# Kernel optimization log

Measured on AMD Instinct MI355X. Metric: run time of the kernel, lower is better.

The kernel has to match this reference:

```python
import jax, jax.numpy as jnp
import numpy as np

B, L, F = 8, 1024, 128
D = 256          # d_model (intermediate_representation)
DI = 512         # d_inner = expand * d_model
N = 32           # d_state
K = 4            # d_conv
R = 16           # dt_rank = ceil(d_model/16)
NC = 2           # n_class


def setup_inputs() -> dict:
    key = jax.random.key(0)
    ks = jax.random.split(key, 12)
    s = 0.02
    return {
        "x": jax.random.normal(ks[0], (B, L, F), jnp.float32),
        "W1": jax.random.normal(ks[1], (D, F), jnp.float32) * s,
        "b1": jnp.zeros((D,), jnp.float32),
        "ln_g": jnp.ones((D,), jnp.float32),
        "ln_b": jnp.zeros((D,), jnp.float32),
        "in_proj_w": jax.random.normal(ks[2], (2 * DI, D), jnp.float32) * s,
        "conv_w": jax.random.normal(ks[3], (DI, K), jnp.float32) * s,
        "conv_b": jnp.zeros((DI,), jnp.float32),
        "x_proj_w": jax.random.normal(ks[4], (R + 2 * N, DI), jnp.float32) * s,
        "dt_proj_w": jax.random.normal(ks[5], (DI, R), jnp.float32) * s,
        "dt_proj_b": jax.random.normal(ks[6], (DI,), jnp.float32) * 0.5,
        "A_log": jnp.log(jnp.broadcast_to(jnp.arange(1, N + 1, dtype=jnp.float32), (DI, N))),
        "D_param": jnp.ones((DI,), jnp.float32),
        "out_proj_w": jax.random.normal(ks[7], (D, DI), jnp.float32) * s,
        "W_out": jax.random.normal(ks[8], (NC, D), jnp.float32) * s,
        "b_out": jnp.zeros((NC,), jnp.float32),
    }


def _mamba(u, in_proj_w, conv_w, conv_b, x_proj_w, dt_proj_w, dt_proj_b, A_log, D_param, out_proj_w):
    # u: (B, L, D)
    xz = u @ in_proj_w.T                      # (B, L, 2*DI)
    xi, z = jnp.split(xz, 2, axis=-1)         # each (B, L, DI)
    # depthwise causal conv1d, kernel K
    xc = jnp.transpose(xi, (0, 2, 1))         # (B, DI, L)
    xc = jax.lax.conv_general_dilated(
        xc, conv_w[:, None, :], (1,), [(K - 1, 0)],
        dimension_numbers=("NCH", "OIH", "NCH"), feature_group_count=DI)
    xi = jnp.transpose(xc, (0, 2, 1)) + conv_b
    xi = jax.nn.silu(xi)
    dbc = xi @ x_proj_w.T                     # (B, L, R+2N)
    dt, Bm, Cm = jnp.split(dbc, [R, R + N], axis=-1)
    delta = jax.nn.softplus(dt @ dt_proj_w.T + dt_proj_b)   # (B, L, DI)
    A = -jnp.exp(A_log)                       # (DI, N)
    dA = jnp.exp(delta[..., None] * A)        # (B, L, DI, N)
    dBu = delta[..., None] * Bm[:, :, None, :] * xi[..., None]  # (B, L, DI, N)

    def step(h, t):
        dA_t, dBu_t, C_t = t
        h = dA_t * h + dBu_t                  # (B, DI, N)
        y = jnp.einsum("bdn,bn->bd", h, C_t)
        return h, y

    h0 = jnp.zeros((u.shape[0], DI, N), u.dtype)
    _, ys = jax.lax.scan(step, h0, (jnp.swapaxes(dA, 0, 1), jnp.swapaxes(dBu, 0, 1), jnp.swapaxes(Cm, 0, 1)))
    y = jnp.swapaxes(ys, 0, 1) + xi * D_param # (B, L, DI)
    y = y * jax.nn.silu(z)
    return y @ out_proj_w.T                   # (B, L, D)


def reference(x, W1, b1, ln_g, ln_b, in_proj_w, conv_w, conv_b, x_proj_w,
              dt_proj_w, dt_proj_b, A_log, D_param, out_proj_w, W_out, b_out):
    h = x @ W1.T + b1                         # (B, L, D)
    mu = jnp.mean(h, -1, keepdims=True)
    var = jnp.var(h, -1, keepdims=True)
    h = (h - mu) / jnp.sqrt(var + 1e-5) * ln_g + ln_b
    h = jax.nn.relu(h)
    h = _mamba(h, in_proj_w, conv_w, conv_b, x_proj_w, dt_proj_w, dt_proj_b,
               A_log, D_param, out_proj_w)
    return h @ W_out.T + b_out                # (B, L, NC)
```

## Files before the change

kernel.cpp:

```cpp
#include <hip/hip_runtime.h>
#include <math.h>

#define BB 8
#define LL 1024
#define FF 128
#define DD 256
#define DIN 512
#define NSTATE 32
#define KCONV 4
#define RNK 16
#define NCLS 2
#define NROWS (BB*LL)
#define NCH 32
#define TCH 32
#define XKS 4
#define XKC (DIN/XKS)

__device__ __forceinline__ unsigned short f2bf(float f) {
  unsigned int x = __float_as_uint(f);
  unsigned int r = (x + 0x7fffu + ((x >> 16) & 1u)) >> 16;
  return (unsigned short)r;
}
__device__ __forceinline__ float bf2f(unsigned short u) {
  return __uint_as_float((unsigned int)u << 16);
}
__device__ __forceinline__ void split_bf(float x, unsigned short& h,
                                         unsigned short& l) {
  h = f2bf(x);
  float hf = __uint_as_float((unsigned int)h << 16);
  l = f2bf(x - hf);
}

typedef __attribute__((ext_vector_type(8))) short frag8;
typedef __attribute__((ext_vector_type(4))) float f32x4;

__global__ __launch_bounds__(256) void head_kernel(
    const float* __restrict__ x, const float* __restrict__ W1,
    const float* __restrict__ b1, const float* __restrict__ ln_g,
    const float* __restrict__ ln_b, unsigned short* __restrict__ u_bf,
    const float* __restrict__ in_proj_w, unsigned short* __restrict__ W_bf,
    const float* __restrict__ W_out, const float* __restrict__ opw,
    float* __restrict__ Wc, const float* __restrict__ xpw,
    unsigned short* __restrict__ xpw_h, unsigned short* __restrict__ xpw_l)
{
  const int blk = blockIdx.x;
  const int tid = threadIdx.x;
  if (blk >= 256) {
    if (blk < 512) {
      int i = (blk - 256) * 256 + tid;
      float4 v = ((const float4*)in_proj_w)[i];
      ushort4 o;
      o.x = f2bf(v.x); o.y = f2bf(v.y); o.z = f2bf(v.z); o.w = f2bf(v.w);
      ((ushort4*)W_bf)[i] = o;
    } else if (blk < 516) {
      int idx = (blk - 512) * 256 + tid;
      int c = idx >> 9;
      int d = idx & (DIN - 1);
      float acc = 0.f;
      for (int j = 0; j < DD; j++)
        acc = fmaf(W_out[c * DD + j], opw[j * DIN + d], acc);
      Wc[idx] = acc;
    } else {
      int i = (blk - 516) * 256 + tid;
      float4 v = ((const float4*)xpw)[i];
      ushort4 hi, lo;
      split_bf(v.x, hi.x, lo.x);
      split_bf(v.y, hi.y, lo.y);
      split_bf(v.z, hi.z, lo.z);
      split_bf(v.w, hi.w, lo.w);
      ((ushort4*)xpw_h)[i] = hi;
      ((ushort4*)xpw_l)[i] = lo;
    }
    return;
  }

  constexpr int BM = 32, BK = 32, K = FF;
  __shared__ __align__(16) unsigned short Ah[BM][40];
  __shared__ __align__(16) unsigned short Al[BM][40];
  __shared__ __align__(16) unsigned short Bh[DD][40];
  __shared__ __align__(16) unsigned short Bl[DD][40];
  __shared__ float srow[2][BM];
  __shared__ float s2row[2][BM];
  const int bm = blk * BM;
  const int wave = tid >> 6;
  const int lane = tid & 63;
  const int lm = lane & 15, quad = lane >> 4;
  const int msub = wave & 1;
  const int ch = wave >> 1;

  f32x4 acc[8];
  #pragma unroll
  for (int j = 0; j < 8; j++) acc[j] = (f32x4){0.f, 0.f, 0.f, 0.f};

  for (int k0 = 0; k0 < K; k0 += BK) {
    {
      int row = tid >> 3, seg = (tid & 7) << 2;
      float4 v = *(const float4*)(x + (size_t)(bm + row) * K + k0 + seg);
      split_bf(v.x, Ah[row][seg + 0], Al[row][seg + 0]);
      split_bf(v.y, Ah[row][seg + 1], Al[row][seg + 1]);
      split_bf(v.z, Ah[row][seg + 2], Al[row][seg + 2]);
      split_bf(v.w, Ah[row][seg + 3], Al[row][seg + 3]);
    }
    #pragma unroll
    for (int it = 0; it < 8; it++) {
      int q = it * 256 + tid;
      int row = q >> 3, seg = (q & 7) << 2;
      float4 v = *(const float4*)(W1 + (size_t)row * K + k0 + seg);
      split_bf(v.x, Bh[row][seg + 0], Bl[row][seg + 0]);
      split_bf(v.y, Bh[row][seg + 1], Bl[row][seg + 1]);
      split_bf(v.z, Bh[row][seg + 2], Bl[row][seg + 2]);
      split_bf(v.w, Bh[row][seg + 3], Bl[row][seg + 3]);
    }
    __syncthreads();
    frag8 ah = *(const frag8*)&Ah[msub * 16 + lm][quad * 8];
    frag8 al = *(const frag8*)&Al[msub * 16 + lm][quad * 8];
    #pragma unroll
    for (int j = 0; j < 8; j++) {
      frag8 bh = *(const frag8*)&Bh[ch * 128 + j * 16 + lm][quad * 8];
      frag8 bl = *(const frag8*)&Bl[ch * 128 + j * 16 + lm][quad * 8];
      acc[j] = __builtin_amdgcn_mfma_f32_16x16x32_bf16(ah, bh, acc[j], 0, 0, 0);
      acc[j] = __builtin_amdgcn_mfma_f32_16x16x32_bf16(ah, bl, acc[j], 0, 0, 0);
      acc[j] = __builtin_amdgcn_mfma_f32_16x16x32_bf16(al, bh, acc[j], 0, 0, 0);
    }
    __syncthreads();
  }

  float b1v[8];
  #pragma unroll
  for (int j = 0; j < 8; j++) b1v[j] = b1[ch * 128 + j * 16 + lm];
  #pragma unroll
  for (int r = 0; r < 4; r++) {
    float s = 0.f, s2 = 0.f;
    #pragma unroll
    for (int j = 0; j < 8; j++) {
      float v = acc[j][r] + b1v[j];
      s += v; s2 = fmaf(v, v, s2);
    }
    s  += __shfl_xor(s, 1);  s  += __shfl_xor(s, 2);
    s  += __shfl_xor(s, 4);  s  += __shfl_xor(s, 8);
    s2 += __shfl_xor(s2, 1); s2 += __shfl_xor(s2, 2);
    s2 += __shfl_xor(s2, 4); s2 += __shfl_xor(s2, 8);
    if (lm == 0) {
      srow[ch][msub * 16 + quad * 4 + r] = s;
      s2row[ch][msub * 16 + quad * 4 + r] = s2;
    }
  }
  __syncthreads();

  float gv[8], bv[8];
  #pragma unroll
  for (int j = 0; j < 8; j++) {
    gv[j] = ln_g[ch * 128 + j * 16 + lm];
    bv[j] = ln_b[ch * 128 + j * 16 + lm];
  }
  #pragma unroll
  for (int r = 0; r < 4; r++) {
    int row32 = msub * 16 + quad * 4 + r;
    float st  = srow[0][row32] + srow[1][row32];
    float s2t = s2row[0][row32] + s2row[1][row32];
    float mean = st * (1.f / DD);
    float var  = s2t * (1.f / DD) - mean * mean;
    float rstd = rsqrtf(var + 1e-5f);
    size_t gr = (size_t)(bm + row32) * DD + ch * 128 + lm;
    #pragma unroll
    for (int j = 0; j < 8; j++) {
      float v = acc[j][r] + b1v[j];
      float o = (v - mean) * rstd * gv[j] + bv[j];
      u_bf[gr + j * 16] = f2bf(o > 0.f ? o : 0.f);
    }
  }
}

__global__ __launch_bounds__(256) void inproj_mfma(
    const unsigned short* __restrict__ A,
    const unsigned short* __restrict__ Bw,
    float* __restrict__ xbuf,
    unsigned short* __restrict__ zbuf)
{
  constexpr int K = DD;
  constexpr int BM = 128, BN = 128, BK = 32;
  __shared__ __align__(16) unsigned short As[BM * BK];
  __shared__ __align__(16) unsigned short Bs[BN * BK];
  const int tid = threadIdx.x;
  const int bm = blockIdx.y * BM;
  const int bn = blockIdx.x * BN;
  const int wave = tid >> 6;
  const int lane = tid & 63;
  const int wm = (wave >> 1) * 64;
  const int wn = (wave & 1) * 64;
  const int lm = lane & 15;
  const int quad = lane >> 4;

  f32x4 acc[4][4];
  #pragma unroll
  for (int i = 0; i < 4; i++)
    #pragma unroll
    for (int j = 0; j < 4; j++)
      acc[i][j] = (f32x4){0.f, 0.f, 0.f, 0.f};

  for (int k0 = 0; k0 < K; k0 += BK) {
    int idx = tid;
    #pragma unroll
    for (int it = 0; it < 2; it++, idx += 256) {
      int row = idx >> 2, seg = (idx & 3) * 8;
      *(uint4*)&As[row * BK + seg] =
          *(const uint4*)&A[(size_t)(bm + row) * K + k0 + seg];
      *(uint4*)&Bs[row * BK + seg] =
          *(const uint4*)&Bw[(size_t)(bn + row) * K + k0 + seg];
    }
    __syncthreads();
    frag8 af[4], bfr[4];
    #pragma unroll
    for (int i = 0; i < 4; i++)
      af[i] = *(const frag8*)&As[(wm + i * 16 + lm) * BK + quad * 8];
    #pragma unroll
    for (int j = 0; j < 4; j++)
      bfr[j] = *(const frag8*)&Bs[(wn + j * 16 + lm) * BK + quad * 8];
    #pragma unroll
    for (int i = 0; i < 4; i++)
      #pragma unroll
      for (int j = 0; j < 4; j++)
        acc[i][j] = __builtin_amdgcn_mfma_f32_16x16x32_bf16(
            af[i], bfr[j], acc[i][j], 0, 0, 0);
    __syncthreads();
  }

  if (bn < DIN) {
    #pragma unroll
    for (int i = 0; i < 4; i++) {
      #pragma unroll
      for (int r = 0; r < 4; r++) {
        int gm = bm + wm + i * 16 + quad * 4 + r;
        float* crow = xbuf + (size_t)gm * DIN + bn + wn + lm;
        #pragma unroll
        for (int j = 0; j < 4; j++)
          crow[j * 16] = acc[i][j][r];
      }
    }
  } else {
    #pragma unroll
    for (int i = 0; i < 4; i++) {
      #pragma unroll
      for (int r = 0; r < 4; r++) {
        int gm = bm + wm + i * 16 + quad * 4 + r;
        unsigned short* zrow = zbuf + (size_t)gm * DIN + (bn - DIN) + wn + lm;
        #pragma unroll
        for (int j = 0; j < 4; j++)
          zrow[j * 16] = f2bf(acc[i][j][r]);
      }
    }
  }
}

__global__ __launch_bounds__(256) void xproj_mfma(
    const float* __restrict__ xbuf, const float* __restrict__ cw,
    const float* __restrict__ cb, const unsigned short* __restrict__ xpw_h,
    const unsigned short* __restrict__ xpw_l,
    float* __restrict__ part, unsigned short* __restrict__ xi_bf)
{
  constexpr int BM = 64;
  __shared__ __align__(16) unsigned short Ah[BM][40];
  __shared__ __align__(16) unsigned short Al[BM][40];
  __shared__ __align__(16) unsigned short Bh[80][40];
  __shared__ __align__(16) unsigned short Bl[80][40];
  const int tid = threadIdx.x;
  const int bm = blockIdx.x * BM;
  const int ks = blockIdx.y;
  const int kb = ks * XKC;
  const int wave = tid >> 6;
  const int lane = tid & 63;
  const int lm = lane & 15, quad = lane >> 4;

  f32x4 acc[5];
  #pragma unroll
  for (int n = 0; n < 5; n++) acc[n] = (f32x4){0.f, 0.f, 0.f, 0.f};

  for (int k0 = 0; k0 < XKC; k0 += 32) {
    for (int q = tid; q < BM * 8; q += 256) {
      int row = q >> 3, seg = (q & 7) << 2;
      int gr = bm + row;
      int l = gr & (LL - 1);
      int dcol = kb + k0 + seg;
      const float* bp = xbuf + (size_t)gr * DIN + dcol;
      float4 c0 = ((const float4*)cw)[dcol + 0];
      float4 c1 = ((const float4*)cw)[dcol + 1];
      float4 c2 = ((const float4*)cw)[dcol + 2];
      float4 c3 = ((const float4*)cw)[dcol + 3];
      float4 a = ((const float4*)cb)[dcol >> 2];
      #pragma unroll
      for (int k = 0; k < KCONV; k++) {
        int lk = l - (KCONV - 1) + k;
        if (lk >= 0) {
          float4 v = *(const float4*)(bp + (ptrdiff_t)(k - (KCONV - 1)) * DIN);
          a.x = fmaf((&c0.x)[k], v.x, a.x);
          a.y = fmaf((&c1.x)[k], v.y, a.y);
          a.z = fmaf((&c2.x)[k], v.z, a.z);
          a.w = fmaf((&c3.x)[k], v.w, a.w);
        }
      }
      float4 r;
      r.x = a.x * (1.f / (1.f + __expf(-a.x)));
      r.y = a.y * (1.f / (1.f + __expf(-a.y)));
      r.z = a.z * (1.f / (1.f + __expf(-a.z)));
      r.w = a.w * (1.f / (1.f + __expf(-a.w)));
      ushort4 xb;
      split_bf(r.x, Ah[row][seg + 0], Al[row][seg + 0]);
      split_bf(r.y, Ah[row][seg + 1], Al[row][seg + 1]);
      split_bf(r.z, Ah[row][seg + 2], Al[row][seg + 2]);
      split_bf(r.w, Ah[row][seg + 3], Al[row][seg + 3]);
      xb.x = Ah[row][seg + 0]; xb.y = Ah[row][seg + 1];
      xb.z = Ah[row][seg + 2]; xb.w = Ah[row][seg + 3];
      *(ushort4*)&xi_bf[(size_t)gr * DIN + dcol] = xb;
    }
    for (int q = tid; q < 80 * 8; q += 256) {
      int row = q >> 3, seg = (q & 7) << 2;
      int g = row * DIN + kb + k0 + seg;
      *(ushort4*)&Bh[row][seg] = *(const ushort4*)&xpw_h[g];
      *(ushort4*)&Bl[row][seg] = *(const ushort4*)&xpw_l[g];
    }
    __syncthreads();
    frag8 ah = *(const frag8*)&Ah[wave * 16 + lm][quad * 8];
    frag8 al = *(const frag8*)&Al[wave * 16 + lm][quad * 8];
    #pragma unroll
    for (int n = 0; n < 5; n++) {
      frag8 bh = *(const frag8*)&Bh[n * 16 + lm][quad * 8];
      frag8 bl = *(const frag8*)&Bl[n * 16 + lm][quad * 8];
      acc[n] = __builtin_amdgcn_mfma_f32_16x16x32_bf16(ah, bh, acc[n], 0, 0, 0);
      acc[n] = __builtin_amdgcn_mfma_f32_16x16x32_bf16(ah, bl, acc[n], 0, 0, 0);
      acc[n] = __builtin_amdgcn_mfma_f32_16x16x32_bf16(al, bh, acc[n], 0, 0, 0);
    }
    __syncthreads();
  }
  #pragma unroll
  for (int n = 0; n < 5; n++) {
    #pragma unroll
    for (int r = 0; r < 4; r++) {
      int gm = bm + wave * 16 + quad * 4 + r;
      part[((size_t)ks * NROWS + gm) * 80 + n * 16 + lm] = acc[n][r];
    }
  }
}

__device__ __forceinline__ float softplus_f(float v) {
  return (v > 20.f) ? v : __logf(1.f + __expf(v));
}

__device__ __forceinline__ void pow_tree(float e1, float* base,
                                         float& e8, float& e16, float& e24) {
  float e2 = e1 * e1;
  float e4 = e2 * e2;
  e8 = e4 * e4;
  e16 = e8 * e8;
  e24 = e16 * e8;
  base[0] = e1;       base[1] = e2;       base[2] = e2 * e1;  base[3] = e4;
  base[4] = e4 * e1;  base[5] = e4 * e2;  base[6] = e4 * base[2]; base[7] = e8;
}

__global__ __launch_bounds__(256) void scan_p1(
    const float* __restrict__ xpart, const unsigned short* __restrict__ xi_bf,
    const float* __restrict__ A_log,
    const float* __restrict__ wdt_g, const float* __restrict__ bdt_g,
    unsigned short* __restrict__ hend, float* __restrict__ sdb,
    float* __restrict__ xsum)
{
  const int blk = blockIdx.x;
  const int half = blk & 1;
  const int c = (blk >> 1) & (NCH - 1);
  const int b = blk >> 6;
  const int tid = threadIdx.x;
  const int d = half * 256 + tid;

  __shared__ float sdbc[TCH * 80];
  {
    const size_t tb = ((size_t)b * LL + c * TCH) * 20;
    const float4* p0 = (const float4*)xpart + tb;
    const float4* p1 = p0 + (size_t)NROWS * 20;
    const float4* p2 = p1 + (size_t)NROWS * 20;
    const float4* p3 = p2 + (size_t)NROWS * 20;
    float4* dst = (float4*)sdbc;
    float4* xs  = (float4*)xsum + tb;
    for (int q = tid; q < TCH * 20; q += 256) {
      float4 a = p0[q], e = p1[q], f = p2[q], g = p3[q];
      float4 o;
      o.x = (a.x + e.x) + (f.x + g.x);
      o.y = (a.y + e.y) + (f.y + g.y);
      o.z = (a.z + e.z) + (f.z + g.z);
      o.w = (a.w + e.w) + (f.w + g.w);
      dst[q] = o;
      if (half == 0) xs[q] = o;
    }
  }

  float h[NSTATE], wdt[16];
  const float A1 = -__expf(A_log[d * NSTATE]);
  #pragma unroll
  for (int n = 0; n < NSTATE; n++) h[n] = 0.f;
  {
    const float4* wp = (const float4*)(wdt_g + d * 16);
    #pragma unroll
    for (int k = 0; k < 4; k++) {
      float4 w = wp[k];
      wdt[4*k+0] = w.x; wdt[4*k+1] = w.y; wdt[4*k+2] = w.z; wdt[4*k+3] = w.w;
    }
  }
  const float bdt = bdt_g[d];
  __syncthreads();

  float sd = 0.f;
  const size_t rowbase = (size_t)b * LL + c * TCH;
  const size_t xib = rowbase * DIN + d;
  float xv_a = bf2f(xi_bf[xib]);
  float xv_b = bf2f(xi_bf[xib + DIN]);
  #pragma unroll 4
  for (int t = 0; t < TCH; t++) {
    float xv = xv_a;
    xv_a = xv_b;
    xv_b = (t + 2 < TCH) ? bf2f(xi_bf[xib + (size_t)(t + 2) * DIN]) : 0.f;
    const float* row = sdbc + t * 80;
    float d0 = bdt, d1 = 0.f, d2 = 0.f, d3 = 0.f;
    #pragma unroll
    for (int j = 0; j < 4; j++) {
      d0 = fmaf(row[j],      wdt[j],      d0);
      d1 = fmaf(row[j + 4],  wdt[j + 4],  d1);
      d2 = fmaf(row[j + 8],  wdt[j + 8],  d2);
      d3 = fmaf(row[j + 12], wdt[j + 12], d3);
    }
    float dtv = (d0 + d1) + (d2 + d3);
    float dlt = softplus_f(dtv);
    float dxv = dlt * xv;
    sd += dlt;
    float base[8], e8, e16, e24;
    pow_tree(__expf(dlt * A1), base, e8, e16, e24);
    #pragma unroll
    for (int k = 0; k < 8; k++) {
      h[k]      = fmaf(base[k],       h[k],      dxv * row[RNK + k]);
      h[k + 8]  = fmaf(base[k] * e8,  h[k + 8],  dxv * row[RNK + k + 8]);
      h[k + 16] = fmaf(base[k] * e16, h[k + 16], dxv * row[RNK + k + 16]);
      h[k + 24] = fmaf(base[k] * e24, h[k + 24], dxv * row[RNK + k + 24]);
    }
  }
  size_t base2 = ((size_t)c * (BB * DIN) + b * DIN + d) * NSTATE;
  ushort4* hv = (ushort4*)(hend + base2);
  #pragma unroll
  for (int k = 0; k < 8; k++) {
    ushort4 o;
    o.x = f2bf(h[4*k]);   o.y = f2bf(h[4*k+1]);
    o.z = f2bf(h[4*k+2]); o.w = f2bf(h[4*k+3]);
    hv[k] = o;
  }
  sdb[c * (BB * DIN) + b * DIN + d] = sd;
}

__global__ __launch_bounds__(256) void scan_p2(
    unsigned short* __restrict__ hend, const float* __restrict__ sdb,
    const float* __restrict__ A_log)
{
  const int idx = blockIdx.x * 256 + threadIdx.x;
  const int n = idx & 31;
  const int pair = idx >> 5;
  const int d = pair & (DIN - 1);
  const float Av = -__expf(A_log[d * NSTATE + n]);
  float h = 0.f;
  size_t off = (size_t)pair * NSTATE + n;
  const size_t stride = (size_t)BB * DIN * NSTATE;
  float he = bf2f(hend[off]);
  float sd = sdb[pair];
  #pragma unroll 1
  for (int c = 0; c < NCH; c++) {
    float he_n = 0.f, sd_n = 0.f;
    if (c + 1 < NCH) {
      he_n = bf2f(hend[off + stride]);
      sd_n = sdb[(size_t)(c + 1) * (BB * DIN) + pair];
    }
    float p = __expf(sd * Av);
    hend[off] = f2bf(h);
    h = fmaf(p, h, he);
    he = he_n; sd = sd_n;
    off += stride;
  }
}

__global__ __launch_bounds__(512) void scan_p3(
    const float* __restrict__ xsum, const unsigned short* __restrict__ xi_bf,
    const unsigned short* __restrict__ zbuf, const float* __restrict__ A_log,
    const float* __restrict__ wdt_g, const float* __restrict__ bdt_g,
    const float* __restrict__ Dp, const float* __restrict__ Wc,
    const float* __restrict__ b_out,
    const unsigned short* __restrict__ hstart, float* __restrict__ out)
{
  const int blk = blockIdx.x;
  const int c = blk & (NCH - 1);
  const int b = blk >> 5;
  const int tid = threadIdx.x;
  const int d = tid;

  __shared__ float sdbc[TCH * 80];
  __shared__ float wcs[2][DIN];
  __shared__ float ymat[16][DIN];
  {
    const size_t tb = ((size_t)b * LL + c * TCH) * 20;
    const float4* p0 = (const float4*)xsum + tb;
    float4* dst = (float4*)sdbc;
    for (int q = tid; q < TCH * 20; q += 512) dst[q] = p0[q];
    wcs[0][tid] = Wc[tid];
    wcs[1][tid] = Wc[DIN + tid];
  }

  float h[NSTATE], wdt[16];
  const float A1 = -__expf(A_log[d * NSTATE]);
  {
    size_t base = ((size_t)c * (BB * DIN) + b * DIN + d) * NSTATE;
    const ushort4* hv = (const ushort4*)(hstart + base);
    #pragma unroll
    for (int k = 0; k < 8; k++) {
      ushort4 v = hv[k];
      h[4*k]   = bf2f(v.x); h[4*k+1] = bf2f(v.y);
      h[4*k+2] = bf2f(v.z); h[4*k+3] = bf2f(v.w);
    }
  }
  {
    const float4* wp = (const float4*)(wdt_g + d * 16);
    #pragma unroll
    for (int k = 0; k < 4; k++) {
      float4 w = wp[k];
      wdt[4*k+0] = w.x; wdt[4*k+1] = w.y; wdt[4*k+2] = w.z; wdt[4*k+3] = w.w;
    }
  }
  const float bdt = bdt_g[d];
  const float Dval = Dp[d];
  __syncthreads();

  const size_t rowbase = (size_t)b * LL + c * TCH;
  const int wave = tid >> 6;
  const int lane = tid & 63;

  #pragma unroll 1
  for (int phase = 0; phase < 2; phase++) {
    const int t0 = phase * 16;
    const size_t xib = (rowbase + t0) * DIN + d;
    float xva = bf2f(xi_bf[xib]);
    float zva = bf2f(zbuf[xib]);
    float xvb = bf2f(xi_bf[xib + DIN]);
    float zvb = bf2f(zbuf[xib + DIN]);
    #pragma unroll 2
    for (int tl = 0; tl < 16; tl++) {
      const int t = t0 + tl;
      float xv = xva, zv = zva;
      xva = xvb; zva = zvb;
      if (tl + 2 < 16) {
        size_t nxt = xib + (size_t)(tl + 2) * DIN;
        xvb = bf2f(xi_bf[nxt]);
        zvb = bf2f(zbuf[nxt]);
      } else { xvb = 0.f; zvb = 0.f; }
      const float* row = sdbc + t * 80;
      float d0 = bdt, d1 = 0.f, d2 = 0.f, d3 = 0.f;
      #pragma unroll
      for (int j = 0; j < 4; j++) {
        d0 = fmaf(row[j],      wdt[j],      d0);
        d1 = fmaf(row[j + 4],  wdt[j + 4],  d1);
        d2 = fmaf(row[j + 8],  wdt[j + 8],  d2);
        d3 = fmaf(row[j + 12], wdt[j + 12], d3);
      }
      float dtv = (d0 + d1) + (d2 + d3);
      float dlt = softplus_f(dtv);
      float dxv = dlt * xv;
      float base[8], e8, e16, e24;
      pow_tree(__expf(dlt * A1), base, e8, e16, e24);
      float yacc = 0.f;
      #pragma unroll
      for (int k = 0; k < 8; k++) {
        h[k]      = fmaf(base[k],       h[k],      dxv * row[RNK + k]);
        h[k + 8]  = fmaf(base[k] * e8,  h[k + 8],  dxv * row[RNK + k + 8]);
        h[k + 16] = fmaf(base[k] * e16, h[k + 16], dxv * row[RNK + k + 16]);
        h[k + 24] = fmaf(base[k] * e24, h[k + 24], dxv * row[RNK + k + 24]);
        yacc = fmaf(h[k],      row[RNK + NSTATE + k],      yacc);
        yacc = fmaf(h[k + 8],  row[RNK + NSTATE + k + 8],  yacc);
        yacc = fmaf(h[k + 16], row[RNK + NSTATE + k + 16], yacc);
        yacc = fmaf(h[k + 24], row[RNK + NSTATE + k + 24], yacc);
      }
      float sg = 1.f / (1.f + __expf(-zv));
      ymat[tl][d] = (yacc + xv * Dval) * (zv * sg);
    }
    __syncthreads();

    #pragma unroll
    for (int i = 0; i < 2; i++) {
      int tl = wave * 2 + i;
      float p0 = 0.f, p1 = 0.f;
      #pragma unroll
      for (int k = 0; k < 8; k++) {
        int dd = lane + k * 64;
        float yv = ymat[tl][dd];
        p0 = fmaf(yv, wcs[0][dd], p0);
        p1 = fmaf(yv, wcs[1][dd], p1);
      }
      #pragma unroll
      for (int off = 32; off > 0; off >>= 1) {
        p0 += __shfl_xor(p0, off);
        p1 += __shfl_xor(p1, off);
      }
      if (lane == 0) {
        out[(rowbase + t0 + tl) * NCLS + 0] = p0 + b_out[0];
        out[(rowbase + t0 + tl) * NCLS + 1] = p1 + b_out[1];
      }
    }
    __syncthreads();
  }
}

extern "C" void kernel_launch(void* const* d_in, const int* in_sizes, int n_in,
                              void* d_out, int out_size, void* d_ws, size_t ws_size,
                              hipStream_t stream)
{
  const float* x         = (const float*)d_in[0];
  const float* W1        = (const float*)d_in[1];
  const float* b1        = (const float*)d_in[2];
  const float* ln_g      = (const float*)d_in[3];
  const float* ln_b      = (const float*)d_in[4];
  const float* in_proj_w = (const float*)d_in[5];
  const float* conv_w    = (const float*)d_in[6];
  const float* conv_b    = (const float*)d_in[7];
  const float* x_proj_w  = (const float*)d_in[8];
  const float* dt_proj_w = (const float*)d_in[9];
  const float* dt_proj_b = (const float*)d_in[10];
  const float* A_log     = (const float*)d_in[11];
  const float* D_param   = (const float*)d_in[12];
  const float* out_proj_w= (const float*)d_in[13];
  const float* W_out     = (const float*)d_in[14];
  const float* b_out     = (const float*)d_in[15];
  float* out = (float*)d_out;

  float* ws   = (float*)d_ws;
  float* xbuf = ws;
  unsigned short* zbuf  = (unsigned short*)(xbuf + (size_t)NROWS * DIN);
  unsigned short* xi_bf = zbuf + (size_t)NROWS * DIN;
  unsigned short* u_bf  = xi_bf + (size_t)NROWS * DIN;
  unsigned short* W_bf  = u_bf + (size_t)NROWS * DD;
  float* Wc    = (float*)(W_bf + 2 * DIN * DD);
  float* sdb   = Wc + 2 * DIN;
  float* xpart = sdb + (size_t)NCH * BB * DIN;
  unsigned short* hend = (unsigned short*)(xpart + (size_t)XKS * NROWS * 80);
  unsigned short* xpw_h = hend + (size_t)NCH * BB * DIN * NSTATE;
  unsigned short* xpw_l = xpw_h + 80 * DIN;
  float* xsum = (float*)(xpw_l + 80 * DIN);

  head_kernel<<<556, 256, 0, stream>>>(x, W1, b1, ln_g, ln_b, u_bf,
                                       in_proj_w, W_bf, W_out, out_proj_w, Wc,
                                       x_proj_w, xpw_h, xpw_l);

  inproj_mfma<<<dim3(8, 64), 256, 0, stream>>>(u_bf, W_bf, xbuf, zbuf);

  xproj_mfma<<<dim3(NROWS / 64, XKS), 256, 0, stream>>>(xbuf, conv_w, conv_b,
                                                        xpw_h, xpw_l, xpart, xi_bf);

  scan_p1<<<BB * NCH * 2, 256, 0, stream>>>(xpart, xi_bf, A_log, dt_proj_w,
                                            dt_proj_b, hend, sdb, xsum);
  scan_p2<<<(BB * DIN * NSTATE) / 256, 256, 0, stream>>>(hend, sdb, A_log);
  scan_p3<<<BB * NCH, 512, 0, stream>>>(xsum, xi_bf, zbuf, A_log, dt_proj_w,
                                        dt_proj_b, D_param, Wc, b_out, hend, out);
}
```

Before: 211.7 us.

## Fuse all six stage kernels into one cooperative persistent kernel with grid syncs

Replaces the separate head, in-projection, x-projection and three scan kernels with one cooperative kernel of 256 blocks of 512 threads. Stages are separated by grid.sync, and each stage uses its own view of a shared-memory union. The goal is to remove the launch gaps and tail effects between the six kernels. In exchange, every stage is forced onto a fixed 256-block grid, so the GEMM stages may lose occupancy and parallelism, and grid-wide barriers add their own cost.

```diff
diff --git a/kernel.cpp b/kernel.cpp
--- a/kernel.cpp
+++ b/kernel.cpp
@@ -1,5 +1,8 @@
 #include <hip/hip_runtime.h>
+#include <hip/hip_cooperative_groups.h>
 #include <math.h>
+
+namespace cg = cooperative_groups;
 
 #define BB 8
 #define LL 1024
@@ -34,313 +37,6 @@
 typedef __attribute__((ext_vector_type(8))) short frag8;
 typedef __attribute__((ext_vector_type(4))) float f32x4;
 
-__global__ __launch_bounds__(256) void head_kernel(
-    const float* __restrict__ x, const float* __restrict__ W1,
-    const float* __restrict__ b1, const float* __restrict__ ln_g,
-    const float* __restrict__ ln_b, unsigned short* __restrict__ u_bf,
-    const float* __restrict__ in_proj_w, unsigned short* __restrict__ W_bf,
-    const float* __restrict__ W_out, const float* __restrict__ opw,
-    float* __restrict__ Wc, const float* __restrict__ xpw,
-    unsigned short* __restrict__ xpw_h, unsigned short* __restrict__ xpw_l)
-{
-  const int blk = blockIdx.x;
-  const int tid = threadIdx.x;
-  if (blk >= 256) {
-    if (blk < 512) {
-      int i = (blk - 256) * 256 + tid;
-      float4 v = ((const float4*)in_proj_w)[i];
-      ushort4 o;
-      o.x = f2bf(v.x); o.y = f2bf(v.y); o.z = f2bf(v.z); o.w = f2bf(v.w);
-      ((ushort4*)W_bf)[i] = o;
-    } else if (blk < 516) {
-      int idx = (blk - 512) * 256 + tid;
-      int c = idx >> 9;
-      int d = idx & (DIN - 1);
-      float acc = 0.f;
-      for (int j = 0; j < DD; j++)
-        acc = fmaf(W_out[c * DD + j], opw[j * DIN + d], acc);
-      Wc[idx] = acc;
-    } else {
-      int i = (blk - 516) * 256 + tid;
-      float4 v = ((const float4*)xpw)[i];
-      ushort4 hi, lo;
-      split_bf(v.x, hi.x, lo.x);
-      split_bf(v.y, hi.y, lo.y);
-      split_bf(v.z, hi.z, lo.z);
-      split_bf(v.w, hi.w, lo.w);
-      ((ushort4*)xpw_h)[i] = hi;
-      ((ushort4*)xpw_l)[i] = lo;
-    }
-    return;
-  }
-
-  constexpr int BM = 32, BK = 32, K = FF;
-  __shared__ __align__(16) unsigned short Ah[BM][40];
-  __shared__ __align__(16) unsigned short Al[BM][40];
-  __shared__ __align__(16) unsigned short Bh[DD][40];
-  __shared__ __align__(16) unsigned short Bl[DD][40];
-  __shared__ float srow[2][BM];
-  __shared__ float s2row[2][BM];
-  const int bm = blk * BM;
-  const int wave = tid >> 6;
-  const int lane = tid & 63;
-  const int lm = lane & 15, quad = lane >> 4;
-  const int msub = wave & 1;
-  const int ch = wave >> 1;
-
-  f32x4 acc[8];
-  #pragma unroll
-  for (int j = 0; j < 8; j++) acc[j] = (f32x4){0.f, 0.f, 0.f, 0.f};
-
-  for (int k0 = 0; k0 < K; k0 += BK) {
-    {
-      int row = tid >> 3, seg = (tid & 7) << 2;
-      float4 v = *(const float4*)(x + (size_t)(bm + row) * K + k0 + seg);
-      split_bf(v.x, Ah[row][seg + 0], Al[row][seg + 0]);
-      split_bf(v.y, Ah[row][seg + 1], Al[row][seg + 1]);
-      split_bf(v.z, Ah[row][seg + 2], Al[row][seg + 2]);
-      split_bf(v.w, Ah[row][seg + 3], Al[row][seg + 3]);
-    }
-    #pragma unroll
-    for (int it = 0; it < 8; it++) {
-      int q = it * 256 + tid;
-      int row = q >> 3, seg = (q & 7) << 2;
-      float4 v = *(const float4*)(W1 + (size_t)row * K + k0 + seg);
-      split_bf(v.x, Bh[row][seg + 0], Bl[row][seg + 0]);
-      split_bf(v.y, Bh[row][seg + 1], Bl[row][seg + 1]);
-      split_bf(v.z, Bh[row][seg + 2], Bl[row][seg + 2]);
-      split_bf(v.w, Bh[row][seg + 3], Bl[row][seg + 3]);
-    }
-    __syncthreads();
-    frag8 ah = *(const frag8*)&Ah[msub * 16 + lm][quad * 8];
-    frag8 al = *(const frag8*)&Al[msub * 16 + lm][quad * 8];
-    #pragma unroll
-    for (int j = 0; j < 8; j++) {
-      frag8 bh = *(const frag8*)&Bh[ch * 128 + j * 16 + lm][quad * 8];
-      frag8 bl = *(const frag8*)&Bl[ch * 128 + j * 16 + lm][quad * 8];
-      acc[j] = __builtin_amdgcn_mfma_f32_16x16x32_bf16(ah, bh, acc[j], 0, 0, 0);
-      acc[j] = __builtin_amdgcn_mfma_f32_16x16x32_bf16(ah, bl, acc[j], 0, 0, 0);
-      acc[j] = __builtin_amdgcn_mfma_f32_16x16x32_bf16(al, bh, acc[j], 0, 0, 0);
-    }
-    __syncthreads();
-  }
-
-  float b1v[8];
-  #pragma unroll
-  for (int j = 0; j < 8; j++) b1v[j] = b1[ch * 128 + j * 16 + lm];
-  #pragma unroll
-  for (int r = 0; r < 4; r++) {
-    float s = 0.f, s2 = 0.f;
-    #pragma unroll
-    for (int j = 0; j < 8; j++) {
-      float v = acc[j][r] + b1v[j];
-      s += v; s2 = fmaf(v, v, s2);
-    }
-    s  += __shfl_xor(s, 1);  s  += __shfl_xor(s, 2);
-    s  += __shfl_xor(s, 4);  s  += __shfl_xor(s, 8);
-    s2 += __shfl_xor(s2, 1); s2 += __shfl_xor(s2, 2);
-    s2 += __shfl_xor(s2, 4); s2 += __shfl_xor(s2, 8);
-    if (lm == 0) {
-      srow[ch][msub * 16 + quad * 4 + r] = s;
-      s2row[ch][msub * 16 + quad * 4 + r] = s2;
-    }
-  }
-  __syncthreads();
-
-  float gv[8], bv[8];
-  #pragma unroll
-  for (int j = 0; j < 8; j++) {
-    gv[j] = ln_g[ch * 128 + j * 16 + lm];
-    bv[j] = ln_b[ch * 128 + j * 16 + lm];
-  }
-  #pragma unroll
-  for (int r = 0; r < 4; r++) {
-    int row32 = msub * 16 + quad * 4 + r;
-    float st  = srow[0][row32] + srow[1][row32];
-    float s2t = s2row[0][row32] + s2row[1][row32];
-    float mean = st * (1.f / DD);
-    float var  = s2t * (1.f / DD) - mean * mean;
-    float rstd = rsqrtf(var + 1e-5f);
-    size_t gr = (size_t)(bm + row32) * DD + ch * 128 + lm;
-    #pragma unroll
-    for (int j = 0; j < 8; j++) {
-      float v = acc[j][r] + b1v[j];
-      float o = (v - mean) * rstd * gv[j] + bv[j];
-      u_bf[gr + j * 16] = f2bf(o > 0.f ? o : 0.f);
-    }
-  }
-}
-
-__global__ __launch_bounds__(256) void inproj_mfma(
-    const unsigned short* __restrict__ A,
-    const unsigned short* __restrict__ Bw,
-    float* __restrict__ xbuf,
-    unsigned short* __restrict__ zbuf)
-{
-  constexpr int K = DD;
-  constexpr int BM = 128, BN = 128, BK = 32;
-  __shared__ __align__(16) unsigned short As[BM * BK];
-  __shared__ __align__(16) unsigned short Bs[BN * BK];
-  const int tid = threadIdx.x;
-  const int bm = blockIdx.y * BM;
-  const int bn = blockIdx.x * BN;
-  const int wave = tid >> 6;
-  const int lane = tid & 63;
-  const int wm = (wave >> 1) * 64;
-  const int wn = (wave & 1) * 64;
-  const int lm = lane & 15;
-  const int quad = lane >> 4;
-
-  f32x4 acc[4][4];
-  #pragma unroll
-  for (int i = 0; i < 4; i++)
-    #pragma unroll
-    for (int j = 0; j < 4; j++)
-      acc[i][j] = (f32x4){0.f, 0.f, 0.f, 0.f};
-
-  for (int k0 = 0; k0 < K; k0 += BK) {
-    int idx = tid;
-    #pragma unroll
-    for (int it = 0; it < 2; it++, idx += 256) {
-      int row = idx >> 2, seg = (idx & 3) * 8;
-      *(uint4*)&As[row * BK + seg] =
-          *(const uint4*)&A[(size_t)(bm + row) * K + k0 + seg];
-      *(uint4*)&Bs[row * BK + seg] =
-          *(const uint4*)&Bw[(size_t)(bn + row) * K + k0 + seg];
-    }
-    __syncthreads();
-    frag8 af[4], bfr[4];
-    #pragma unroll
-    for (int i = 0; i < 4; i++)
-      af[i] = *(const frag8*)&As[(wm + i * 16 + lm) * BK + quad * 8];
-    #pragma unroll
-    for (int j = 0; j < 4; j++)
-      bfr[j] = *(const frag8*)&Bs[(wn + j * 16 + lm) * BK + quad * 8];
-    #pragma unroll
-    for (int i = 0; i < 4; i++)
-      #pragma unroll
-      for (int j = 0; j < 4; j++)
-        acc[i][j] = __builtin_amdgcn_mfma_f32_16x16x32_bf16(
-            af[i], bfr[j], acc[i][j], 0, 0, 0);
-    __syncthreads();
-  }
-
-  if (bn < DIN) {
-    #pragma unroll
-    for (int i = 0; i < 4; i++) {
-      #pragma unroll
-      for (int r = 0; r < 4; r++) {
-        int gm = bm + wm + i * 16 + quad * 4 + r;
-        float* crow = xbuf + (size_t)gm * DIN + bn + wn + lm;
-        #pragma unroll
-        for (int j = 0; j < 4; j++)
-          crow[j * 16] = acc[i][j][r];
-      }
-    }
-  } else {
-    #pragma unroll
-    for (int i = 0; i < 4; i++) {
-      #pragma unroll
-      for (int r = 0; r < 4; r++) {
-        int gm = bm + wm + i * 16 + quad * 4 + r;
-        unsigned short* zrow = zbuf + (size_t)gm * DIN + (bn - DIN) + wn + lm;
-        #pragma unroll
-        for (int j = 0; j < 4; j++)
-          zrow[j * 16] = f2bf(acc[i][j][r]);
-      }
-    }
-  }
-}
-
-__global__ __launch_bounds__(256) void xproj_mfma(
-    const float* __restrict__ xbuf, const float* __restrict__ cw,
-    const float* __restrict__ cb, const unsigned short* __restrict__ xpw_h,
-    const unsigned short* __restrict__ xpw_l,
-    float* __restrict__ part, unsigned short* __restrict__ xi_bf)
-{
-  constexpr int BM = 64;
-  __shared__ __align__(16) unsigned short Ah[BM][40];
-  __shared__ __align__(16) unsigned short Al[BM][40];
-  __shared__ __align__(16) unsigned short Bh[80][40];
-  __shared__ __align__(16) unsigned short Bl[80][40];
-  const int tid = threadIdx.x;
-  const int bm = blockIdx.x * BM;
-  const int ks = blockIdx.y;
-  const int kb = ks * XKC;
-  const int wave = tid >> 6;
-  const int lane = tid & 63;
-  const int lm = lane & 15, quad = lane >> 4;
-
-  f32x4 acc[5];
-  #pragma unroll
-  for (int n = 0; n < 5; n++) acc[n] = (f32x4){0.f, 0.f, 0.f, 0.f};
-
-  for (int k0 = 0; k0 < XKC; k0 += 32) {
-    for (int q = tid; q < BM * 8; q += 256) {
-      int row = q >> 3, seg = (q & 7) << 2;
-      int gr = bm + row;
-      int l = gr & (LL - 1);
-      int dcol = kb + k0 + seg;
-      const float* bp = xbuf + (size_t)gr * DIN + dcol;
-      float4 c0 = ((const float4*)cw)[dcol + 0];
-      float4 c1 = ((const float4*)cw)[dcol + 1];
-      float4 c2 = ((const float4*)cw)[dcol + 2];
-      float4 c3 = ((const float4*)cw)[dcol + 3];
-      float4 a = ((const float4*)cb)[dcol >> 2];
-      #pragma unroll
-      for (int k = 0; k < KCONV; k++) {
-        int lk = l - (KCONV - 1) + k;
-        if (lk >= 0) {
-          float4 v = *(const float4*)(bp + (ptrdiff_t)(k - (KCONV - 1)) * DIN);
-          a.x = fmaf((&c0.x)[k], v.x, a.x);
-          a.y = fmaf((&c1.x)[k], v.y, a.y);
-          a.z = fmaf((&c2.x)[k], v.z, a.z);
-          a.w = fmaf((&c3.x)[k], v.w, a.w);
-        }
-      }
-      float4 r;
-      r.x = a.x * (1.f / (1.f + __expf(-a.x)));
-      r.y = a.y * (1.f / (1.f + __expf(-a.y)));
-      r.z = a.z * (1.f / (1.f + __expf(-a.z)));
-      r.w = a.w * (1.f / (1.f + __expf(-a.w)));
-      ushort4 xb;
-      split_bf(r.x, Ah[row][seg + 0], Al[row][seg + 0]);
-      split_bf(r.y, Ah[row][seg + 1], Al[row][seg + 1]);
-      split_bf(r.z, Ah[row][seg + 2], Al[row][seg + 2]);
-      split_bf(r.w, Ah[row][seg + 3], Al[row][seg + 3]);
-      xb.x = Ah[row][seg + 0]; xb.y = Ah[row][seg + 1];
-      xb.z = Ah[row][seg + 2]; xb.w = Ah[row][seg + 3];
-      *(ushort4*)&xi_bf[(size_t)gr * DIN + dcol] = xb;
-    }
-    for (int q = tid; q < 80 * 8; q += 256) {
-      int row = q >> 3, seg = (q & 7) << 2;
-      int g = row * DIN + kb + k0 + seg;
-      *(ushort4*)&Bh[row][seg] = *(const ushort4*)&xpw_h[g];
-      *(ushort4*)&Bl[row][seg] = *(const ushort4*)&xpw_l[g];
-    }
-    __syncthreads();
-    frag8 ah = *(const frag8*)&Ah[wave * 16 + lm][quad * 8];
-    frag8 al = *(const frag8*)&Al[wave * 16 + lm][quad * 8];
-    #pragma unroll
-    for (int n = 0; n < 5; n++) {
-      frag8 bh = *(const frag8*)&Bh[n * 16 + lm][quad * 8];
-      frag8 bl = *(const frag8*)&Bl[n * 16 + lm][quad * 8];
-      acc[n] = __builtin_amdgcn_mfma_f32_16x16x32_bf16(ah, bh, acc[n], 0, 0, 0);
-      acc[n] = __builtin_amdgcn_mfma_f32_16x16x32_bf16(ah, bl, acc[n], 0, 0, 0);
-      acc[n] = __builtin_amdgcn_mfma_f32_16x16x32_bf16(al, bh, acc[n], 0, 0, 0);
-    }
-    __syncthreads();
-  }
-  #pragma unroll
-  for (int n = 0; n < 5; n++) {
-    #pragma unroll
-    for (int r = 0; r < 4; r++) {
-      int gm = bm + wave * 16 + quad * 4 + r;
-      part[((size_t)ks * NROWS + gm) * 80 + n * 16 + lm] = acc[n][r];
-    }
-  }
-}
-
 __device__ __forceinline__ float softplus_f(float v) {
   return (v > 20.f) ? v : __logf(1.f + __expf(v));
 }
@@ -356,203 +52,346 @@
   base[4] = e4 * e1;  base[5] = e4 * e2;  base[6] = e4 * base[2]; base[7] = e8;
 }
 
-__global__ __launch_bounds__(256) void scan_p1(
-    const float* __restrict__ xpart, const unsigned short* __restrict__ xi_bf,
-    const float* __restrict__ A_log,
-    const float* __restrict__ wdt_g, const float* __restrict__ bdt_g,
-    unsigned short* __restrict__ hend, float* __restrict__ sdb,
-    float* __restrict__ xsum)
+struct MegaArgs {
+  const float *x, *W1, *b1, *ln_g, *ln_b, *in_proj_w, *conv_w, *conv_b,
+              *x_proj_w, *dt_proj_w, *dt_proj_b, *A_log, *D_param,
+              *out_proj_w, *W_out, *b_out;
+  float* out;
+  float* xbuf;
+  unsigned short *zbuf, *xi_bf, *u_bf, *W_bf;
+  float *Wc, *sdb, *xpart;
+  unsigned short *hend, *xpw_h, *xpw_l;
+};
+
+union __align__(16) SMem {
+  struct { unsigned short Ah[64][40], Al[64][40], Bh[256][40], Bl[256][40];
+           float srow[2][64], s2row[2][64]; } hd;
+  struct { unsigned short As[128*32], Bs[256*32]; } ip;
+  struct { unsigned short Ah[128][40], Al[128][40],
+           Bh[80][40], Bl[80][40]; } xp;
+  struct { float sdbc[TCH*80];
+           float wcs[2][DIN]; float ymat[16][DIN]; } sc;
+};
+
+__global__ __launch_bounds__(512, 2) void mega(MegaArgs a)
 {
+  cg::grid_group grid = cg::this_grid();
+  __shared__ SMem sm;
   const int blk = blockIdx.x;
-  const int half = blk & 1;
-  const int c = (blk >> 1) & (NCH - 1);
-  const int b = blk >> 6;
   const int tid = threadIdx.x;
-  const int d = half * 256 + tid;
-
-  __shared__ float sdbc[TCH * 80];
-  {
-    const size_t tb = ((size_t)b * LL + c * TCH) * 20;
-    const float4* p0 = (const float4*)xpart + tb;
-    const float4* p1 = p0 + (size_t)NROWS * 20;
-    const float4* p2 = p1 + (size_t)NROWS * 20;
-    const float4* p3 = p2 + (size_t)NROWS * 20;
-    float4* dst = (float4*)sdbc;
-    float4* xs  = (float4*)xsum + tb;
-    for (int q = tid; q < TCH * 20; q += 256) {
-      float4 a = p0[q], e = p1[q], f = p2[q], g = p3[q];
-      float4 o;
-      o.x = (a.x + e.x) + (f.x + g.x);
-      o.y = (a.y + e.y) + (f.y + g.y);
-      o.z = (a.z + e.z) + (f.z + g.z);
-      o.w = (a.w + e.w) + (f.w + g.w);
-      dst[q] = o;
-      if (half == 0) xs[q] = o;
-    }
-  }
-
-  float h[NSTATE], wdt[16];
-  const float A1 = -__expf(A_log[d * NSTATE]);
-  #pragma unroll
-  for (int n = 0; n < NSTATE; n++) h[n] = 0.f;
-  {
-    const float4* wp = (const float4*)(wdt_g + d * 16);
-    #pragma unroll
-    for (int k = 0; k < 4; k++) {
-      float4 w = wp[k];
-      wdt[4*k+0] = w.x; wdt[4*k+1] = w.y; wdt[4*k+2] = w.z; wdt[4*k+3] = w.w;
-    }
-  }
-  const float bdt = bdt_g[d];
-  __syncthreads();
-
-  float sd = 0.f;
-  const size_t rowbase = (size_t)b * LL + c * TCH;
-  const size_t xib = rowbase * DIN + d;
-  float xv_a = bf2f(xi_bf[xib]);
-  float xv_b = bf2f(xi_bf[xib + DIN]);
-  #pragma unroll 4
-  for (int t = 0; t < TCH; t++) {
-    float xv = xv_a;
-    xv_a = xv_b;
-    xv_b = (t + 2 < TCH) ? bf2f(xi_bf[xib + (size_t)(t + 2) * DIN]) : 0.f;
-    const float* row = sdbc + t * 80;
-    float d0 = bdt, d1 = 0.f, d2 = 0.f, d3 = 0.f;
-    #pragma unroll
-    for (int j = 0; j < 4; j++) {
-      d0 = fmaf(row[j],      wdt[j],      d0);
-      d1 = fmaf(row[j + 4],  wdt[j + 4],  d1);
-      d2 = fmaf(row[j + 8],  wdt[j + 8],  d2);
-      d3 = fmaf(row[j + 12], wdt[j + 12], d3);
-    }
-    float dtv = (d0 + d1) + (d2 + d3);
-    float dlt = softplus_f(dtv);
-    float dxv = dlt * xv;
-    sd += dlt;
-    float base[8], e8, e16, e24;
-    pow_tree(__expf(dlt * A1), base, e8, e16, e24);
-    #pragma unroll
-    for (int k = 0; k < 8; k++) {
-      h[k]      = fmaf(base[k],       h[k],      dxv * row[RNK + k]);
-      h[k + 8]  = fmaf(base[k] * e8,  h[k + 8],  dxv * row[RNK + k + 8]);
-      h[k + 16] = fmaf(base[k] * e16, h[k + 16], dxv * row[RNK + k + 16]);
-      h[k + 24] = fmaf(base[k] * e24, h[k + 24], dxv * row[RNK + k + 24]);
-    }
-  }
-  size_t base2 = ((size_t)c * (BB * DIN) + b * DIN + d) * NSTATE;
-  ushort4* hv = (ushort4*)(hend + base2);
-  #pragma unroll
-  for (int k = 0; k < 8; k++) {
-    ushort4 o;
-    o.x = f2bf(h[4*k]);   o.y = f2bf(h[4*k+1]);
-    o.z = f2bf(h[4*k+2]); o.w = f2bf(h[4*k+3]);
-    hv[k] = o;
-  }
-  sdb[c * (BB * DIN) + b * DIN + d] = sd;
-}
-
-__global__ __launch_bounds__(256) void scan_p2(
-    unsigned short* __restrict__ hend, const float* __restrict__ sdb,
-    const float* __restrict__ A_log)
-{
-  const int idx = blockIdx.x * 256 + threadIdx.x;
-  const int n = idx & 31;
-  const int pair = idx >> 5;
-  const int d = pair & (DIN - 1);
-  const float Av = -__expf(A_log[d * NSTATE + n]);
-  float h = 0.f;
-  size_t off = (size_t)pair * NSTATE + n;
-  const size_t stride = (size_t)BB * DIN * NSTATE;
-  float he = bf2f(hend[off]);
-  float sd = sdb[pair];
-  #pragma unroll 1
-  for (int c = 0; c < NCH; c++) {
-    float he_n = 0.f, sd_n = 0.f;
-    if (c + 1 < NCH) {
-      he_n = bf2f(hend[off + stride]);
-      sd_n = sdb[(size_t)(c + 1) * (BB * DIN) + pair];
-    }
-    float p = __expf(sd * Av);
-    hend[off] = f2bf(h);
-    h = fmaf(p, h, he);
-    he = he_n; sd = sd_n;
-    off += stride;
-  }
-}
-
-__global__ __launch_bounds__(512) void scan_p3(
-    const float* __restrict__ xsum, const unsigned short* __restrict__ xi_bf,
-    const unsigned short* __restrict__ zbuf, const float* __restrict__ A_log,
-    const float* __restrict__ wdt_g, const float* __restrict__ bdt_g,
-    const float* __restrict__ Dp, const float* __restrict__ Wc,
-    const float* __restrict__ b_out,
-    const unsigned short* __restrict__ hstart, float* __restrict__ out)
-{
-  const int blk = blockIdx.x;
-  const int c = blk & (NCH - 1);
-  const int b = blk >> 5;
-  const int tid = threadIdx.x;
-  const int d = tid;
-
-  __shared__ float sdbc[TCH * 80];
-  __shared__ float wcs[2][DIN];
-  __shared__ float ymat[16][DIN];
-  {
-    const size_t tb = ((size_t)b * LL + c * TCH) * 20;
-    const float4* p0 = (const float4*)xsum + tb;
-    float4* dst = (float4*)sdbc;
-    for (int q = tid; q < TCH * 20; q += 512) dst[q] = p0[q];
-    wcs[0][tid] = Wc[tid];
-    wcs[1][tid] = Wc[DIN + tid];
-  }
-
-  float h[NSTATE], wdt[16];
-  const float A1 = -__expf(A_log[d * NSTATE]);
-  {
-    size_t base = ((size_t)c * (BB * DIN) + b * DIN + d) * NSTATE;
-    const ushort4* hv = (const ushort4*)(hstart + base);
-    #pragma unroll
-    for (int k = 0; k < 8; k++) {
-      ushort4 v = hv[k];
-      h[4*k]   = bf2f(v.x); h[4*k+1] = bf2f(v.y);
-      h[4*k+2] = bf2f(v.z); h[4*k+3] = bf2f(v.w);
-    }
-  }
-  {
-    const float4* wp = (const float4*)(wdt_g + d * 16);
-    #pragma unroll
-    for (int k = 0; k < 4; k++) {
-      float4 w = wp[k];
-      wdt[4*k+0] = w.x; wdt[4*k+1] = w.y; wdt[4*k+2] = w.z; wdt[4*k+3] = w.w;
-    }
-  }
-  const float bdt = bdt_g[d];
-  const float Dval = Dp[d];
-  __syncthreads();
-
-  const size_t rowbase = (size_t)b * LL + c * TCH;
   const int wave = tid >> 6;
   const int lane = tid & 63;
-
-  #pragma unroll 1
-  for (int phase = 0; phase < 2; phase++) {
-    const int t0 = phase * 16;
-    const size_t xib = (rowbase + t0) * DIN + d;
-    float xva = bf2f(xi_bf[xib]);
-    float zva = bf2f(zbuf[xib]);
-    float xvb = bf2f(xi_bf[xib + DIN]);
-    float zvb = bf2f(zbuf[xib + DIN]);
-    #pragma unroll 2
-    for (int tl = 0; tl < 16; tl++) {
-      const int t = t0 + tl;
-      float xv = xva, zv = zva;
-      xva = xvb; zva = zvb;
-      if (tl + 2 < 16) {
-        size_t nxt = xib + (size_t)(tl + 2) * DIN;
-        xvb = bf2f(xi_bf[nxt]);
-        zvb = bf2f(zbuf[nxt]);
-      } else { xvb = 0.f; zvb = 0.f; }
-      const float* row = sdbc + t * 80;
+  const int lm = lane & 15, quad = lane >> 4;
+
+  if (blk < 128) {
+    const int bm = blk * 64;
+    const int msub = wave & 3;
+    const int ch = wave >> 2;
+    f32x4 acc[8];
+    #pragma unroll
+    for (int j = 0; j < 8; j++) acc[j] = (f32x4){0.f, 0.f, 0.f, 0.f};
+
+    for (int k0 = 0; k0 < FF; k0 += 32) {
+      {
+        int row = tid >> 3, seg = (tid & 7) << 2;
+        float4 v = *(const float4*)(a.x + (size_t)(bm + row) * FF + k0 + seg);
+        split_bf(v.x, sm.hd.Ah[row][seg + 0], sm.hd.Al[row][seg + 0]);
+        split_bf(v.y, sm.hd.Ah[row][seg + 1], sm.hd.Al[row][seg + 1]);
+        split_bf(v.z, sm.hd.Ah[row][seg + 2], sm.hd.Al[row][seg + 2]);
+        split_bf(v.w, sm.hd.Ah[row][seg + 3], sm.hd.Al[row][seg + 3]);
+      }
+      #pragma unroll
+      for (int it = 0; it < 4; it++) {
+        int q = it * 512 + tid;
+        int row = q >> 3, seg = (q & 7) << 2;
+        float4 v = *(const float4*)(a.W1 + (size_t)row * FF + k0 + seg);
+        split_bf(v.x, sm.hd.Bh[row][seg + 0], sm.hd.Bl[row][seg + 0]);
+        split_bf(v.y, sm.hd.Bh[row][seg + 1], sm.hd.Bl[row][seg + 1]);
+        split_bf(v.z, sm.hd.Bh[row][seg + 2], sm.hd.Bl[row][seg + 2]);
+        split_bf(v.w, sm.hd.Bh[row][seg + 3], sm.hd.Bl[row][seg + 3]);
+      }
+      __syncthreads();
+      frag8 ah = *(const frag8*)&sm.hd.Ah[msub * 16 + lm][quad * 8];
+      frag8 al = *(const frag8*)&sm.hd.Al[msub * 16 + lm][quad * 8];
+      #pragma unroll
+      for (int j = 0; j < 8; j++) {
+        frag8 bh = *(const frag8*)&sm.hd.Bh[ch * 128 + j * 16 + lm][quad * 8];
+        frag8 bl = *(const frag8*)&sm.hd.Bl[ch * 128 + j * 16 + lm][quad * 8];
+        acc[j] = __builtin_amdgcn_mfma_f32_16x16x32_bf16(ah, bh, acc[j], 0, 0, 0);
+        acc[j] = __builtin_amdgcn_mfma_f32_16x16x32_bf16(ah, bl, acc[j], 0, 0, 0);
+        acc[j] = __builtin_amdgcn_mfma_f32_16x16x32_bf16(al, bh, acc[j], 0, 0, 0);
+      }
+      __syncthreads();
+    }
+
+    float b1v[8];
+    #pragma unroll
+    for (int j = 0; j < 8; j++) b1v[j] = a.b1[ch * 128 + j * 16 + lm];
+    #pragma unroll
+    for (int r = 0; r < 4; r++) {
+      float s = 0.f, s2 = 0.f;
+      #pragma unroll
+      for (int j = 0; j < 8; j++) {
+        float v = acc[j][r] + b1v[j];
+        s += v; s2 = fmaf(v, v, s2);
+      }
+      s  += __shfl_xor(s, 1);  s  += __shfl_xor(s, 2);
+      s  += __shfl_xor(s, 4);  s  += __shfl_xor(s, 8);
+      s2 += __shfl_xor(s2, 1); s2 += __shfl_xor(s2, 2);
+      s2 += __shfl_xor(s2, 4); s2 += __shfl_xor(s2, 8);
+      if (lm == 0) {
+        sm.hd.srow[ch][msub * 16 + quad * 4 + r] = s;
+        sm.hd.s2row[ch][msub * 16 + quad * 4 + r] = s2;
+      }
+    }
+    __syncthreads();
+
+    float gv[8], bv[8];
+    #pragma unroll
+    for (int j = 0; j < 8; j++) {
+      gv[j] = a.ln_g[ch * 128 + j * 16 + lm];
+      bv[j] = a.ln_b[ch * 128 + j * 16 + lm];
+    }
+    #pragma unroll
+    for (int r = 0; r < 4; r++) {
+      int row64 = msub * 16 + quad * 4 + r;
+      float st  = sm.hd.srow[0][row64] + sm.hd.srow[1][row64];
+      float s2t = sm.hd.s2row[0][row64] + sm.hd.s2row[1][row64];
+      float mean = st * (1.f / DD);
+      float var  = s2t * (1.f / DD) - mean * mean;
+      float rstd = rsqrtf(var + 1e-5f);
+      size_t gr = (size_t)(bm + row64) * DD + ch * 128 + lm;
+      #pragma unroll
+      for (int j = 0; j < 8; j++) {
+        float v = acc[j][r] + b1v[j];
+        float o = (v - mean) * rstd * gv[j] + bv[j];
+        a.u_bf[gr + j * 16] = f2bf(o > 0.f ? o : 0.f);
+      }
+    }
+  } else if (blk < 192) {
+    int base = (blk - 128) * 1024 + tid;
+    #pragma unroll
+    for (int it = 0; it < 2; it++) {
+      int i = base + it * 512;
+      float4 v = ((const float4*)a.in_proj_w)[i];
+      ushort4 o;
+      o.x = f2bf(v.x); o.y = f2bf(v.y); o.z = f2bf(v.z); o.w = f2bf(v.w);
+      ((ushort4*)a.W_bf)[i] = o;
+    }
+  } else if (blk < 194) {
+    int idx = (blk - 192) * 512 + tid;
+    int cc = idx >> 9;
+    int dd = idx & (DIN - 1);
+    float s = 0.f;
+    for (int j = 0; j < DD; j++)
+      s = fmaf(a.W_out[cc * DD + j], a.out_proj_w[j * DIN + dd], s);
+    a.Wc[idx] = s;
+  } else if (blk < 214) {
+    int i = (blk - 194) * 512 + tid;
+    float4 v = ((const float4*)a.x_proj_w)[i];
+    ushort4 hi, lo;
+    split_bf(v.x, hi.x, lo.x);
+    split_bf(v.y, hi.y, lo.y);
+    split_bf(v.z, hi.z, lo.z);
+    split_bf(v.w, hi.w, lo.w);
+    ((ushort4*)a.xpw_h)[i] = hi;
+    ((ushort4*)a.xpw_l)[i] = lo;
+  }
+  grid.sync();
+
+  {
+    const int bn = (blk & 3) * 256;
+    const int bm = (blk >> 2) * 128;
+    const int wm = (wave >> 2) * 64;
+    const int wn = (wave & 3) * 64;
+    f32x4 acc[4][4];
+    #pragma unroll
+    for (int i = 0; i < 4; i++)
+      #pragma unroll
+      for (int j = 0; j < 4; j++)
+        acc[i][j] = (f32x4){0.f, 0.f, 0.f, 0.f};
+
+    for (int k0 = 0; k0 < DD; k0 += 32) {
+      {
+        int row = tid >> 2, seg = (tid & 3) * 8;
+        *(uint4*)&sm.ip.As[row * 32 + seg] =
+            *(const uint4*)&a.u_bf[(size_t)(bm + row) * DD + k0 + seg];
+      }
+      #pragma unroll
+      for (int it = 0; it < 2; it++) {
+        int q = it * 512 + tid;
+        int row = q >> 2, seg = (q & 3) * 8;
+        *(uint4*)&sm.ip.Bs[row * 32 + seg] =
+            *(const uint4*)&a.W_bf[(size_t)(bn + row) * DD + k0 + seg];
+      }
+      __syncthreads();
+      frag8 af[4], bfr[4];
+      #pragma unroll
+      for (int i = 0; i < 4; i++)
+        af[i] = *(const frag8*)&sm.ip.As[(wm + i * 16 + lm) * 32 + quad * 8];
+      #pragma unroll
+      for (int j = 0; j < 4; j++)
+        bfr[j] = *(const frag8*)&sm.ip.Bs[(wn + j * 16 + lm) * 32 + quad * 8];
+      #pragma unroll
+      for (int i = 0; i < 4; i++)
+        #pragma unroll
+        for (int j = 0; j < 4; j++)
+          acc[i][j] = __builtin_amdgcn_mfma_f32_16x16x32_bf16(
+              af[i], bfr[j], acc[i][j], 0, 0, 0);
+      __syncthreads();
+    }
+
+    if (bn < DIN) {
+      #pragma unroll
+      for (int i = 0; i < 4; i++) {
+        #pragma unroll
+        for (int r = 0; r < 4; r++) {
+          int gm = bm + wm + i * 16 + quad * 4 + r;
+          float* crow = a.xbuf + (size_t)gm * DIN + bn + wn + lm;
+          #pragma unroll
+          for (int j = 0; j < 4; j++)
+            crow[j * 16] = acc[i][j][r];
+        }
+      }
+    } else {
+      #pragma unroll
+      for (int i = 0; i < 4; i++) {
+        #pragma unroll
+        for (int r = 0; r < 4; r++) {
+          int gm = bm + wm + i * 16 + quad * 4 + r;
+          unsigned short* zrow = a.zbuf + (size_t)gm * DIN + (bn - DIN) + wn + lm;
+          #pragma unroll
+          for (int j = 0; j < 4; j++)
+            zrow[j * 16] = f2bf(acc[i][j][r]);
+        }
+      }
+    }
+  }
+  grid.sync();
+
+  {
+    const int ks = blk & 3;
+    const int bm = (blk >> 2) * 128;
+    const int kb = ks * XKC;
+    f32x4 acc[5];
+    #pragma unroll
+    for (int n = 0; n < 5; n++) acc[n] = (f32x4){0.f, 0.f, 0.f, 0.f};
+
+    for (int k0 = 0; k0 < XKC; k0 += 32) {
+      for (int q = tid; q < 128 * 8; q += 512) {
+        int row = q >> 3, seg = (q & 7) << 2;
+        int gr = bm + row;
+        int l = gr & (LL - 1);
+        int dcol = kb + k0 + seg;
+        const float* bp = a.xbuf + (size_t)gr * DIN + dcol;
+        float4 c0 = ((const float4*)a.conv_w)[dcol + 0];
+        float4 c1 = ((const float4*)a.conv_w)[dcol + 1];
+        float4 c2 = ((const float4*)a.conv_w)[dcol + 2];
+        float4 c3 = ((const float4*)a.conv_w)[dcol + 3];
+        float4 ac = ((const float4*)a.conv_b)[dcol >> 2];
+        #pragma unroll
+        for (int k = 0; k < KCONV; k++) {
+          int lk = l - (KCONV - 1) + k;
+          if (lk >= 0) {
+            float4 v = *(const float4*)(bp + (ptrdiff_t)(k - (KCONV - 1)) * DIN);
+            ac.x = fmaf((&c0.x)[k], v.x, ac.x);
+            ac.y = fmaf((&c1.x)[k], v.y, ac.y);
+            ac.z = fmaf((&c2.x)[k], v.z, ac.z);
+            ac.w = fmaf((&c3.x)[k], v.w, ac.w);
+          }
+        }
+        float4 r;
+        r.x = ac.x * (1.f / (1.f + __expf(-ac.x)));
+        r.y = ac.y * (1.f / (1.f + __expf(-ac.y)));
+        r.z = ac.z * (1.f / (1.f + __expf(-ac.z)));
+        r.w = ac.w * (1.f / (1.f + __expf(-ac.w)));
+        ushort4 xb;
+        split_bf(r.x, sm.xp.Ah[row][seg + 0], sm.xp.Al[row][seg + 0]);
+        split_bf(r.y, sm.xp.Ah[row][seg + 1], sm.xp.Al[row][seg + 1]);
+        split_bf(r.z, sm.xp.Ah[row][seg + 2], sm.xp.Al[row][seg + 2]);
+        split_bf(r.w, sm.xp.Ah[row][seg + 3], sm.xp.Al[row][seg + 3]);
+        xb.x = sm.xp.Ah[row][seg + 0]; xb.y = sm.xp.Ah[row][seg + 1];
+        xb.z = sm.xp.Ah[row][seg + 2]; xb.w = sm.xp.Ah[row][seg + 3];
+        *(ushort4*)&a.xi_bf[(size_t)gr * DIN + dcol] = xb;
+      }
+      for (int q = tid; q < 80 * 8; q += 512) {
+        int row = q >> 3, seg = (q & 7) << 2;
+        int g = row * DIN + kb + k0 + seg;
+        *(ushort4*)&sm.xp.Bh[row][seg] = *(const ushort4*)&a.xpw_h[g];
+        *(ushort4*)&sm.xp.Bl[row][seg] = *(const ushort4*)&a.xpw_l[g];
+      }
+      __syncthreads();
+      frag8 ah = *(const frag8*)&sm.xp.Ah[wave * 16 + lm][quad * 8];
+      frag8 al = *(const frag8*)&sm.xp.Al[wave * 16 + lm][quad * 8];
+      #pragma unroll
+      for (int n = 0; n < 5; n++) {
+        frag8 bh = *(const frag8*)&sm.xp.Bh[n * 16 + lm][quad * 8];
+        frag8 bl = *(const frag8*)&sm.xp.Bl[n * 16 + lm][quad * 8];
+        acc[n] = __builtin_amdgcn_mfma_f32_16x16x32_bf16(ah, bh, acc[n], 0, 0, 0);
+        acc[n] = __builtin_amdgcn_mfma_f32_16x16x32_bf16(ah, bl, acc[n], 0, 0, 0);
+        acc[n] = __builtin_amdgcn_mfma_f32_16x16x32_bf16(al, bh, acc[n], 0, 0, 0);
+      }
+      __syncthreads();
+    }
+    #pragma unroll
+    for (int n = 0; n < 5; n++) {
+      #pragma unroll
+      for (int r = 0; r < 4; r++) {
+        int gm = bm + wave * 16 + quad * 4 + r;
+        a.xpart[((size_t)ks * NROWS + gm) * 80 + n * 16 + lm] = acc[n][r];
+      }
+    }
+  }
+  grid.sync();
+
+  {
+    const int c = blk & (NCH - 1);
+    const int b = blk >> 5;
+    const int d = tid;
+    {
+      const size_t tb = ((size_t)b * LL + c * TCH) * 20;
+      const float4* p0 = (const float4*)a.xpart + tb;
+      const float4* p1 = p0 + (size_t)NROWS * 20;
+      const float4* p2 = p1 + (size_t)NROWS * 20;
+      const float4* p3 = p2 + (size_t)NROWS * 20;
+      float4* dst = (float4*)sm.sc.sdbc;
+      for (int q = tid; q < TCH * 20; q += 512) {
+        float4 va = p0[q], e = p1[q], f = p2[q], g = p3[q];
+        float4 o;
+        o.x = (va.x + e.x) + (f.x + g.x);
+        o.y = (va.y + e.y) + (f.y + g.y);
+        o.z = (va.z + e.z) + (f.z + g.z);
+        o.w = (va.w + e.w) + (f.w + g.w);
+        dst[q] = o;
+      }
+    }
+
+    float h[NSTATE], wdt[16];
+    const float A1 = -__expf(a.A_log[d * NSTATE]);
+    #pragma unroll
+    for (int n = 0; n < NSTATE; n++) h[n] = 0.f;
+    {
+      const float4* wp = (const float4*)(a.dt_proj_w + d * 16);
+      #pragma unroll
+      for (int k = 0; k < 4; k++) {
+        float4 w = wp[k];
+        wdt[4*k+0] = w.x; wdt[4*k+1] = w.y; wdt[4*k+2] = w.z; wdt[4*k+3] = w.w;
+      }
+    }
+    const float bdt = a.dt_proj_b[d];
+    __syncthreads();
+
+    float sd = 0.f;
+    const size_t rowbase = (size_t)b * LL + c * TCH;
+    const size_t xib = rowbase * DIN + d;
+    float xv_a = bf2f(a.xi_bf[xib]);
+    float xv_b = bf2f(a.xi_bf[xib + DIN]);
+    #pragma unroll 4
+    for (int t = 0; t < TCH; t++) {
+      float xv = xv_a;
+      xv_a = xv_b;
+      xv_b = (t + 2 < TCH) ? bf2f(a.xi_bf[xib + (size_t)(t + 2) * DIN]) : 0.f;
+      const float* row = sm.sc.sdbc + t * 80;
       float d0 = bdt, d1 = 0.f, d2 = 0.f, d3 = 0.f;
       #pragma unroll
       for (int j = 0; j < 4; j++) {
@@ -564,47 +403,163 @@
       float dtv = (d0 + d1) + (d2 + d3);
       float dlt = softplus_f(dtv);
       float dxv = dlt * xv;
+      sd += dlt;
       float base[8], e8, e16, e24;
       pow_tree(__expf(dlt * A1), base, e8, e16, e24);
-      float yacc = 0.f;
       #pragma unroll
       for (int k = 0; k < 8; k++) {
         h[k]      = fmaf(base[k],       h[k],      dxv * row[RNK + k]);
         h[k + 8]  = fmaf(base[k] * e8,  h[k + 8],  dxv * row[RNK + k + 8]);
         h[k + 16] = fmaf(base[k] * e16, h[k + 16], dxv * row[RNK + k + 16]);
         h[k + 24] = fmaf(base[k] * e24, h[k + 24], dxv * row[RNK + k + 24]);
-        yacc = fmaf(h[k],      row[RNK + NSTATE + k],      yacc);
-        yacc = fmaf(h[k + 8],  row[RNK + NSTATE + k + 8],  yacc);
-        yacc = fmaf(h[k + 16], row[RNK + NSTATE + k + 16], yacc);
-        yacc = fmaf(h[k + 24], row[RNK + NSTATE + k + 24], yacc);
-      }
-      float sg = 1.f / (1.f + __expf(-zv));
-      ymat[tl][d] = (yacc + xv * Dval) * (zv * sg);
-    }
+      }
+    }
+    size_t base2 = ((size_t)c * (BB * DIN) + b * DIN + d) * NSTATE;
+    ushort4* hv = (ushort4*)(a.hend + base2);
+    #pragma unroll
+    for (int k = 0; k < 8; k++) {
+      ushort4 o;
+      o.x = f2bf(h[4*k]);   o.y = f2bf(h[4*k+1]);
+      o.z = f2bf(h[4*k+2]); o.w = f2bf(h[4*k+3]);
+      hv[k] = o;
+    }
+    a.sdb[c * (BB * DIN) + b * DIN + d] = sd;
+  }
+  grid.sync();
+
+  {
+    const int idx = blk * 512 + tid;
+    const int n = idx & 31;
+    const int pair = idx >> 5;
+    const int d = pair & (DIN - 1);
+    const float Av = -__expf(a.A_log[d * NSTATE + n]);
+    float h = 0.f;
+    size_t off = (size_t)pair * NSTATE + n;
+    const size_t stride = (size_t)BB * DIN * NSTATE;
+    float he = bf2f(a.hend[off]);
+    float sd = a.sdb[pair];
+    #pragma unroll 1
+    for (int c = 0; c < NCH; c++) {
+      float he_n = 0.f, sd_n = 0.f;
+      if (c + 1 < NCH) {
+        he_n = bf2f(a.hend[off + stride]);
+        sd_n = a.sdb[(size_t)(c + 1) * (BB * DIN) + pair];
+      }
+      float p = __expf(sd * Av);
+      a.hend[off] = f2bf(h);
+      h = fmaf(p, h, he);
+      he = he_n; sd = sd_n;
+      off += stride;
+    }
+  }
+  grid.sync();
+
+  {
+    const int c = blk & (NCH - 1);
+    const int b = blk >> 5;
+    const int d = tid;
+
+    sm.sc.wcs[0][tid] = a.Wc[tid];
+    sm.sc.wcs[1][tid] = a.Wc[DIN + tid];
+
+    float h[NSTATE], wdt[16];
+    const float A1 = -__expf(a.A_log[d * NSTATE]);
+    {
+      size_t base = ((size_t)c * (BB * DIN) + b * DIN + d) * NSTATE;
+      const ushort4* hv = (const ushort4*)(a.hend + base);
+      #pragma unroll
+      for (int k = 0; k < 8; k++) {
+        ushort4 v = hv[k];
+        h[4*k]   = bf2f(v.x); h[4*k+1] = bf2f(v.y);
+        h[4*k+2] = bf2f(v.z); h[4*k+3] = bf2f(v.w);
+      }
+    }
+    {
+      const float4* wp = (const float4*)(a.dt_proj_w + d * 16);
+      #pragma unroll
+      for (int k = 0; k < 4; k++) {
+        float4 w = wp[k];
+        wdt[4*k+0] = w.x; wdt[4*k+1] = w.y; wdt[4*k+2] = w.z; wdt[4*k+3] = w.w;
+      }
+    }
+    const float bdt = a.dt_proj_b[d];
+    const float Dval = a.D_param[d];
     __syncthreads();
 
-    #pragma unroll
-    for (int i = 0; i < 2; i++) {
-      int tl = wave * 2 + i;
-      float p0 = 0.f, p1 = 0.f;
-      #pragma unroll
-      for (int k = 0; k < 8; k++) {
-        int dd = lane + k * 64;
-        float yv = ymat[tl][dd];
-        p0 = fmaf(yv, wcs[0][dd], p0);
-        p1 = fmaf(yv, wcs[1][dd], p1);
-      }
-      #pragma unroll
-      for (int off = 32; off > 0; off >>= 1) {
-        p0 += __shfl_xor(p0, off);
-        p1 += __shfl_xor(p1, off);
-      }
-      if (lane == 0) {
-        out[(rowbase + t0 + tl) * NCLS + 0] = p0 + b_out[0];
-        out[(rowbase + t0 + tl) * NCLS + 1] = p1 + b_out[1];
-      }
-    }
-    __syncthreads();
+    const size_t rowbase = (size_t)b * LL + c * TCH;
+
+    #pragma unroll 1
+    for (int phase = 0; phase < 2; phase++) {
+      const int t0 = phase * 16;
+      const size_t xib = (rowbase + t0) * DIN + d;
+      float xva = bf2f(a.xi_bf[xib]);
+      float zva = bf2f(a.zbuf[xib]);
+      float xvb = bf2f(a.xi_bf[xib + DIN]);
+      float zvb = bf2f(a.zbuf[xib + DIN]);
+      #pragma unroll 2
+      for (int tl = 0; tl < 16; tl++) {
+        const int t = t0 + tl;
+        float xv = xva, zv = zva;
+        xva = xvb; zva = zvb;
+        if (tl + 2 < 16) {
+          size_t nxt = xib + (size_t)(tl + 2) * DIN;
+          xvb = bf2f(a.xi_bf[nxt]);
+          zvb = bf2f(a.zbuf[nxt]);
+        } else { xvb = 0.f; zvb = 0.f; }
+        const float* row = sm.sc.sdbc + t * 80;
+        float d0 = bdt, d1 = 0.f, d2 = 0.f, d3 = 0.f;
+        #pragma unroll
+        for (int j = 0; j < 4; j++) {
+          d0 = fmaf(row[j],      wdt[j],      d0);
+          d1 = fmaf(row[j + 4],  wdt[j + 4],  d1);
+          d2 = fmaf(row[j + 8],  wdt[j + 8],  d2);
+          d3 = fmaf(row[j + 12], wdt[j + 12], d3);
+        }
+        float dtv = (d0 + d1) + (d2 + d3);
+        float dlt = softplus_f(dtv);
+        float dxv = dlt * xv;
+        float base[8], e8, e16, e24;
+        pow_tree(__expf(dlt * A1), base, e8, e16, e24);
+        float yacc = 0.f;
+        #pragma unroll
+        for (int k = 0; k < 8; k++) {
+          h[k]      = fmaf(base[k],       h[k],      dxv * row[RNK + k]);
+          h[k + 8]  = fmaf(base[k] * e8,  h[k + 8],  dxv * row[RNK + k + 8]);
+          h[k + 16] = fmaf(base[k] * e16, h[k + 16], dxv * row[RNK + k + 16]);
+          h[k + 24] = fmaf(base[k] * e24, h[k + 24], dxv * row[RNK + k + 24]);
+          yacc = fmaf(h[k],      row[RNK + NSTATE + k],      yacc);
+          yacc = fmaf(h[k + 8],  row[RNK + NSTATE + k + 8],  yacc);
+          yacc = fmaf(h[k + 16], row[RNK + NSTATE + k + 16], yacc);
+          yacc = fmaf(h[k + 24], row[RNK + NSTATE + k + 24], yacc);
+        }
+        float sg = 1.f / (1.f + __expf(-zv));
+        sm.sc.ymat[tl][d] = (yacc + xv * Dval) * (zv * sg);
+      }
+      __syncthreads();
+
+      #pragma unroll
+      for (int i = 0; i < 2; i++) {
+        int tl = wave * 2 + i;
+        float p0 = 0.f, p1 = 0.f;
+        #pragma unroll
+        for (int k = 0; k < 8; k++) {
+          int dd = lane + k * 64;
+          float yv = sm.sc.ymat[tl][dd];
+          p0 = fmaf(yv, sm.sc.wcs[0][dd], p0);
+          p1 = fmaf(yv, sm.sc.wcs[1][dd], p1);
+        }
+        #pragma unroll
+        for (int off = 32; off > 0; off >>= 1) {
+          p0 += __shfl_xor(p0, off);
+          p1 += __shfl_xor(p1, off);
+        }
+        if (lane == 0) {
+          a.out[(rowbase + t0 + tl) * NCLS + 0] = p0 + a.b_out[0];
+          a.out[(rowbase + t0 + tl) * NCLS + 1] = p1 + a.b_out[1];
+        }
+      }
+      __syncthreads();
+    }
   }
 }
 
@@ -612,24 +567,6 @@
                               void* d_out, int out_size, void* d_ws, size_t ws_size,
                               hipStream_t stream)
 {
-  const float* x         = (const float*)d_in[0];
-  const float* W1        = (const float*)d_in[1];
-  const float* b1        = (const float*)d_in[2];
-  const float* ln_g      = (const float*)d_in[3];
-  const float* ln_b      = (const float*)d_in[4];
-  const float* in_proj_w = (const float*)d_in[5];
-  const float* conv_w    = (const float*)d_in[6];
-  const float* conv_b    = (const float*)d_in[7];
-  const float* x_proj_w  = (const float*)d_in[8];
-  const float* dt_proj_w = (const float*)d_in[9];
-  const float* dt_proj_b = (const float*)d_in[10];
-  const float* A_log     = (const float*)d_in[11];
-  const float* D_param   = (const float*)d_in[12];
-  const float* out_proj_w= (const float*)d_in[13];
-  const float* W_out     = (const float*)d_in[14];
-  const float* b_out     = (const float*)d_in[15];
-  float* out = (float*)d_out;
-
   float* ws   = (float*)d_ws;
   float* xbuf = ws;
   unsigned short* zbuf  = (unsigned short*)(xbuf + (size_t)NROWS * DIN);
@@ -642,20 +579,30 @@
   unsigned short* hend = (unsigned short*)(xpart + (size_t)XKS * NROWS * 80);
   unsigned short* xpw_h = hend + (size_t)NCH * BB * DIN * NSTATE;
   unsigned short* xpw_l = xpw_h + 80 * DIN;
-  float* xsum = (float*)(xpw_l + 80 * DIN);
-
-  head_kernel<<<556, 256, 0, stream>>>(x, W1, b1, ln_g, ln_b, u_bf,
-                                       in_proj_w, W_bf, W_out, out_proj_w, Wc,
-                                       x_proj_w, xpw_h, xpw_l);
-
-  inproj_mfma<<<dim3(8, 64), 256, 0, stream>>>(u_bf, W_bf, xbuf, zbuf);
-
-  xproj_mfma<<<dim3(NROWS / 64, XKS), 256, 0, stream>>>(xbuf, conv_w, conv_b,
-                                                        xpw_h, xpw_l, xpart, xi_bf);
-
-  scan_p1<<<BB * NCH * 2, 256, 0, stream>>>(xpart, xi_bf, A_log, dt_proj_w,
-                                            dt_proj_b, hend, sdb, xsum);
-  scan_p2<<<(BB * DIN * NSTATE) / 256, 256, 0, stream>>>(hend, sdb, A_log);
-  scan_p3<<<BB * NCH, 512, 0, stream>>>(xsum, xi_bf, zbuf, A_log, dt_proj_w,
-                                        dt_proj_b, D_param, Wc, b_out, hend, out);
+
+  MegaArgs a;
+  a.x         = (const float*)d_in[0];
+  a.W1        = (const float*)d_in[1];
+  a.b1        = (const float*)d_in[2];
+  a.ln_g      = (const float*)d_in[3];
+  a.ln_b      = (const float*)d_in[4];
+  a.in_proj_w = (const float*)d_in[5];
+  a.conv_w    = (const float*)d_in[6];
+  a.conv_b    = (const float*)d_in[7];
+  a.x_proj_w  = (const float*)d_in[8];
+  a.dt_proj_w = (const float*)d_in[9];
+  a.dt_proj_b = (const float*)d_in[10];
+  a.A_log     = (const float*)d_in[11];
+  a.D_param   = (const float*)d_in[12];
+  a.out_proj_w= (const float*)d_in[13];
+  a.W_out     = (const float*)d_in[14];
+  a.b_out     = (const float*)d_in[15];
+  a.out   = (float*)d_out;
+  a.xbuf  = xbuf;  a.zbuf = zbuf;  a.xi_bf = xi_bf;  a.u_bf = u_bf;
+  a.W_bf  = W_bf;  a.Wc = Wc;      a.sdb = sdb;      a.xpart = xpart;
+  a.hend  = hend;  a.xpw_h = xpw_h; a.xpw_l = xpw_l;
+
+  void* kp[] = { (void*)&a };
+  hipLaunchCooperativeKernel((const void*)mega, dim3(BB * NCH), dim3(512),
+                             kp, 0, stream);
 }
```

New measurement: 399.8 us. 88.8% more time.
